# Kernel tuning notes

Hardware: AMD Instinct MI355X
Metric: run time of the kernel (lower is better)

## Reference

```python
import jax, jax.numpy as jnp
import numpy as np

N = 50000   # nodes
E = 800000  # edges
D = 128     # nfeat == nhid
C = 40      # nclass
L = 4       # nlayer
EPS_BN = 1e-5
EPS_PN = 1e-6
PN_SCALE = 1.0


def setup_inputs() -> dict:
    key = jax.random.key(0)
    ks = jax.random.split(key, 10)
    x = jax.random.normal(ks[0], (N, D), jnp.float32)
    edge_row = jax.random.randint(ks[1], (E,), 0, N)   # destination rows of adj
    edge_col = jax.random.randint(ks[2], (E,), 0, N)   # source cols of adj
    edge_val = jax.random.uniform(ks[3], (E,), jnp.float32)
    # BatchNorm1d(nfeat) affine params
    bn_gamma = jnp.ones((D,), jnp.float32)
    bn_beta = jnp.zeros((D,), jnp.float32)
    s = 1.0 / np.sqrt(D)
    fc_in_w = jax.random.uniform(ks[4], (D, D), jnp.float32, -s, s)
    fc_in_b = jax.random.uniform(ks[5], (D,), jnp.float32, -s, s)
    gc_w = jax.random.uniform(ks[6], (L, D, D), jnp.float32, -s, s)
    gc_b = jax.random.uniform(ks[7], (L, D), jnp.float32, -s, s)
    fc_out_w = jax.random.uniform(ks[8], (D, C), jnp.float32, -s, s)
    fc_out_b = jax.random.uniform(ks[9], (C,), jnp.float32, -s, s)
    return dict(x=x, edge_row=edge_row, edge_col=edge_col, edge_val=edge_val,
                bn_gamma=bn_gamma, bn_beta=bn_beta,
                fc_in_w=fc_in_w, fc_in_b=fc_in_b,
                gc_w=gc_w, gc_b=gc_b,
                fc_out_w=fc_out_w, fc_out_b=fc_out_b)


def pair_norm(x):
    # PairNorm 'PN': center columns, scale by sqrt(mean row squared-norm)
    x = x - x.mean(axis=0, keepdims=True)
    rownorm_mean = jnp.sqrt(EPS_PN + jnp.mean(jnp.sum(x * x, axis=1)))
    return PN_SCALE * x / rownorm_mean


def spmm(edge_row, edge_col, edge_val, h):
    # out[i] = sum_{e: row(e)=i} val_e * h[col(e)]  (torch.spmm(adj, h))
    return jax.ops.segment_sum(edge_val[:, None] * h[edge_col], edge_row, num_segments=N)


def reference(x, edge_row, edge_col, edge_val, bn_gamma, bn_beta,
              fc_in_w, fc_in_b, gc_w, gc_b, fc_out_w, fc_out_b):
    x_old = jnp.zeros_like(x)  # zeros_like(input x), shape [N, D]
    # BatchNorm1d over nodes (batch statistics; dropout inactive / eval)
    mu = x.mean(axis=0)
    var = x.var(axis=0)
    x = (x - mu) / jnp.sqrt(var + EPS_BN) * bn_gamma + bn_beta
    x = x @ fc_in_w + fc_in_b
    for i in range(L):
        h = x @ gc_w[i]                                   # [N, D] dense GEMM
        h = spmm(edge_row, edge_col, edge_val, h) + gc_b[i]
        h = jax.nn.relu(pair_norm(h))
        # skip=1 -> i % 1 == 0 always: residual add every layer
        x = h + x_old
        x_old = x
    return x @ fc_out_w + fc_out_b
```

## Files before the change

kernel.cpp:

```cpp
#include <hip/hip_runtime.h>
#include <hip/hip_bf16.h>


constexpr int DD = 128;

struct alignas(16) f4 { float v[4]; };
typedef unsigned short ushort;
typedef unsigned int uint;
typedef short short8 __attribute__((ext_vector_type(8)));
typedef float f32x4 __attribute__((ext_vector_type(4)));

__device__ inline ushort f2bf(float f) {
    uint u = __float_as_uint(f);
    u += 0x7fffu + ((u >> 16) & 1u);
    return (ushort)(u >> 16);
}
__device__ inline void bf8_unpack(uint4 u, float* v) {
    v[0] = __uint_as_float(u.x << 16); v[1] = __uint_as_float(u.x & 0xffff0000u);
    v[2] = __uint_as_float(u.y << 16); v[3] = __uint_as_float(u.y & 0xffff0000u);
    v[4] = __uint_as_float(u.z << 16); v[5] = __uint_as_float(u.z & 0xffff0000u);
    v[6] = __uint_as_float(u.w << 16); v[7] = __uint_as_float(u.w & 0xffff0000u);
}
__device__ inline uint4 bf8_pack(const float* v) {
    uint4 o;
    o.x = (uint)f2bf(v[0]) | ((uint)f2bf(v[1]) << 16);
    o.y = (uint)f2bf(v[2]) | ((uint)f2bf(v[3]) << 16);
    o.z = (uint)f2bf(v[4]) | ((uint)f2bf(v[5]) << 16);
    o.w = (uint)f2bf(v[6]) | ((uint)f2bf(v[7]) << 16);
    return o;
}

__global__ __launch_bounds__(256) void col_reduce_k(const float* __restrict__ X, int n,
    float* __restrict__ psum, float* __restrict__ psq)
{
    int c = threadIdx.x & (DD - 1);
    int half = threadIdx.x >> 7;
    int rows_per_blk = (n + gridDim.x - 1) / gridDim.x;
    int r0 = blockIdx.x * rows_per_blk;
    int r1 = min(n, r0 + rows_per_blk);
    float s = 0.f, ss = 0.f;
    for (int r = r0 + half; r < r1; r += 2) {
        float v = X[(size_t)r * DD + c];
        s += v; ss += v * v;
    }
    __shared__ float ls[256], lq[256];
    ls[threadIdx.x] = s; lq[threadIdx.x] = ss;
    __syncthreads();
    if (half == 0) {
        psum[blockIdx.x * DD + c] = ls[c] + ls[c + 128];
        psq [blockIdx.x * DD + c] = lq[c] + lq[c + 128];
    }
}

template<bool BN>
__global__ __launch_bounds__(1024) void finalize_k(const float* __restrict__ psum,
    const float* __restrict__ psq, int nblk, int n,
    const float* __restrict__ gamma, const float* __restrict__ beta,
    float* __restrict__ AB)
{
    const int c = threadIdx.x & (DD - 1);
    const int g = threadIdx.x >> 7;
    float s = 0.f, ss = 0.f;
    for (int b = g; b < nblk; b += 8) {
        s  += psum[b * DD + c];
        ss += psq [b * DD + c];
    }
    __shared__ float Ls[8][DD], Lq[8][DD];
    Ls[g][c] = s; Lq[g][c] = ss;
    __syncthreads();
    float ts = 0.f, tss = 0.f;
    #pragma unroll
    for (int k = 0; k < 8; k++) { ts += Ls[k][c]; tss += Lq[k][c]; }
    float mu = ts / (float)n;
    if (BN) {
        if (threadIdx.x < DD) {
            float var = tss / (float)n - mu * mu;
            float a = gamma[c] * rsqrtf(var + 1e-5f);
            AB[c] = a;
            AB[DD + c] = beta[c] - mu * a;
        }
    } else {
        float cent = tss - (float)n * mu * mu;
        __syncthreads();
        if (g == 0) Ls[0][c] = cent;
        __syncthreads();
        for (int off = 64; off > 0; off >>= 1) {
            if (threadIdx.x < off) Ls[0][threadIdx.x] += Ls[0][threadIdx.x + off];
            __syncthreads();
        }
        if (threadIdx.x < DD) {
            float inv = rsqrtf(1e-6f + Ls[0][0] / (float)n);
            AB[c] = inv;
            AB[DD + c] = -mu * inv;
        }
    }
}

__global__ __launch_bounds__(256) void weights_k(const float* __restrict__ gc_w,
    const float* __restrict__ fc_in_w, const float* __restrict__ fc_in_b,
    const float* __restrict__ fc_out_w,
    ushort* __restrict__ Wt, ushort* __restrict__ Wtc, ushort* __restrict__ WtO,
    float* __restrict__ bc)
{
    const int b = blockIdx.x;
    const int t = threadIdx.x;
    if (b < 64) {
        int w = b >> 4, tile = b & 15;
        int tr = (tile >> 2) * 32, tc = (tile & 3) * 32;
        const float* W = gc_w + (size_t)w * DD * DD;
        ushort* Wo = Wt + (size_t)w * DD * DD;
        __shared__ float tls[32][33];
        int tx = t & 31, ty = t >> 5;
        #pragma unroll
        for (int j = 0; j < 32; j += 8)
            tls[ty + j][tx] = W[(size_t)(tr + ty + j) * DD + tc + tx];
        __syncthreads();
        #pragma unroll
        for (int j = 0; j < 32; j += 8)
            Wo[(size_t)(tc + ty + j) * DD + (tr + tx)] = f2bf(tls[tx][ty + j]);
    } else if (b == 64) {
        for (int i = t; i < 48 * DD; i += 256) {
            int nn = i >> 7, k = i & 127;
            float v = (nn < 40) ? fc_out_w[(size_t)k * 40 + nn] : 0.f;
            WtO[i] = f2bf(v);
        }
    } else if (b == 65) {
        if (t < DD) {
            float acc = 0.f;
            for (int j = 0; j < DD; j++) acc += fc_in_b[j] * gc_w[(size_t)j * DD + t];
            bc[t] = acc;
        }
    } else {
        int idx = (b - 66) * 256 + t;
        int nn = idx & 127, k = idx >> 7;
        float acc = 0.f;
        for (int j = 0; j < DD; j++)
            acc += fc_in_w[(size_t)k * DD + j] * gc_w[(size_t)j * DD + nn];
        Wtc[(size_t)nn * DD + k] = f2bf(acc);
    }
}

template<int PRE, int NCOLF, int NCOLW, bool BIAS, bool OUTBF, bool WRITEX>
__global__ __launch_bounds__(256) void gemm_mfma_k(const void* __restrict__ INv,
    const ushort* __restrict__ Wt, const float* __restrict__ AB,
    const float* __restrict__ bias, void* __restrict__ Xresv,
    void* __restrict__ Yout, int ystride, int n)
{
    __shared__ short xs[128][136];
    __shared__ short ws[NCOLF * 16][136];
    __shared__ float bias_s[DD];
    const int t = threadIdx.x;
    if (BIAS && t < NCOLW) bias_s[t] = bias[t];

    const int row0 = blockIdx.x * 128;
    if (PRE <= 1) {
        const float* IN = (const float*)INv;
        for (int i = t; i < 128 * 32; i += 256) {
            int m = i >> 5, koff = (i & 31) << 2;
            int r = row0 + m;
            f4 v; v.v[0] = v.v[1] = v.v[2] = v.v[3] = 0.f;
            if (r < n) {
                v = *reinterpret_cast<const f4*>(IN + (size_t)r * DD + koff);
                #pragma unroll
                for (int j = 0; j < 4; j++) v.v[j] = v.v[j] * AB[koff + j] + AB[DD + koff + j];
            }
            uint2 p;
            p.x = (uint)f2bf(v.v[0]) | ((uint)f2bf(v.v[1]) << 16);
            p.y = (uint)f2bf(v.v[2]) | ((uint)f2bf(v.v[3]) << 16);
            *reinterpret_cast<uint2*>(&xs[m][koff]) = p;
        }
    } else {
        const ushort* IN = (const ushort*)INv;
        ushort* Xres = (ushort*)Xresv;
        for (int i = t; i < 128 * 16; i += 256) {
            int m = i >> 4, k8 = (i & 15) << 3;
            int r = row0 + m;
            float v[8];
            if (r < n) {
                uint4 u = *reinterpret_cast<const uint4*>(IN + (size_t)r * DD + k8);
                bf8_unpack(u, v);
                #pragma unroll
                for (int j = 0; j < 8; j++)
                    v[j] = fmaxf(v[j] * AB[k8 + j] + AB[DD + k8 + j], 0.f);
                if (PRE == 3) {
                    uint4 xo = *reinterpret_cast<const uint4*>(Xres + (size_t)r * DD + k8);
                    float xov[8]; bf8_unpack(xo, xov);
                    #pragma unroll
                    for (int j = 0; j < 8; j++) v[j] += xov[j];
                }
                uint4 pk = bf8_pack(v);
                if (WRITEX)
                    *reinterpret_cast<uint4*>(Xres + (size_t)r * DD + k8) = pk;
                *reinterpret_cast<uint4*>(&xs[m][k8]) = pk;
            } else {
                uint4 z; z.x = z.y = z.z = z.w = 0u;
                *reinterpret_cast<uint4*>(&xs[m][k8]) = z;
            }
        }
    }
    for (int i = t; i < NCOLF * 256; i += 256) {
        int nn = i >> 4, koff = (i & 15) << 3;
        *reinterpret_cast<uint4*>(&ws[nn][koff]) =
            *reinterpret_cast<const uint4*>(Wt + (size_t)nn * DD + koff);
    }
    __syncthreads();

    const int wave = t >> 6, lane = t & 63, fr = lane & 15, g = lane >> 4;
    f32x4 acc[2][NCOLF];
    #pragma unroll
    for (int m = 0; m < 2; m++)
        #pragma unroll
        for (int c = 0; c < NCOLF; c++) acc[m][c] = (f32x4){0.f, 0.f, 0.f, 0.f};

    #pragma unroll 2
    for (int ks = 0; ks < 4; ks++) {
        int k0 = ks * 32 + g * 8;
        short8 a0 = *reinterpret_cast<const short8*>(&xs[wave * 32 + fr][k0]);
        short8 a1 = *reinterpret_cast<const short8*>(&xs[wave * 32 + 16 + fr][k0]);
        #pragma unroll
        for (int c = 0; c < NCOLF; c++) {
            short8 b = *reinterpret_cast<const short8*>(&ws[c * 16 + fr][k0]);
            acc[0][c] = __builtin_amdgcn_mfma_f32_16x16x32_bf16(b, a0, acc[0][c], 0, 0, 0);
            acc[1][c] = __builtin_amdgcn_mfma_f32_16x16x32_bf16(b, a1, acc[1][c], 0, 0, 0);
        }
    }

    #pragma unroll
    for (int m = 0; m < 2; m++) {
        const int row = row0 + wave * 32 + m * 16 + fr;
        if (row < n) {
            #pragma unroll
            for (int c = 0; c < NCOLF; c++) {
                int n0 = c * 16 + g * 4;
                if (OUTBF) {
                    float b0 = BIAS ? bias_s[n0 + 0] : 0.f, b1 = BIAS ? bias_s[n0 + 1] : 0.f;
                    float b2 = BIAS ? bias_s[n0 + 2] : 0.f, b3 = BIAS ? bias_s[n0 + 3] : 0.f;
                    uint2 o;
                    o.x = (uint)f2bf(acc[m][c][0] + b0) | ((uint)f2bf(acc[m][c][1] + b1) << 16);
                    o.y = (uint)f2bf(acc[m][c][2] + b2) | ((uint)f2bf(acc[m][c][3] + b3) << 16);
                    *reinterpret_cast<uint2*>((ushort*)Yout + (size_t)row * DD + n0) = o;
                } else if (n0 + 3 < NCOLW) {
                    f4 o;
                    #pragma unroll
                    for (int j = 0; j < 4; j++)
                        o.v[j] = acc[m][c][j] + (BIAS ? bias_s[n0 + j] : 0.f);
                    *reinterpret_cast<f4*>((float*)Yout + (size_t)row * ystride + n0) = o;
                }
            }
        }
    }
}

__global__ __launch_bounds__(256) void hist_k(const int* __restrict__ erow,
    int* __restrict__ deg, int e)
{
    int i = blockIdx.x * 256 + threadIdx.x;
    if (i < e) atomicAdd(&deg[erow[i]], 1);
}

constexpr int SCAN_TILE = 1024;
constexpr int BSH = 9;

__global__ __launch_bounds__(256) void scan1_k(const int* __restrict__ deg,
    int* __restrict__ local, int* __restrict__ bsum, int n)
{
    const int t = threadIdx.x;
    const int base = blockIdx.x * SCAN_TILE + t * 4;
    int v0 = 0, v1 = 0, v2 = 0, v3 = 0;
    if (base + 3 < n) {
        int4 v = *reinterpret_cast<const int4*>(deg + base);
        v0 = v.x; v1 = v.y; v2 = v.z; v3 = v.w;
    } else {
        if (base + 0 < n) v0 = deg[base + 0];
        if (base + 1 < n) v1 = deg[base + 1];
        if (base + 2 < n) v2 = deg[base + 2];
        if (base + 3 < n) v3 = deg[base + 3];
    }
    int s = v0 + v1 + v2 + v3;
    __shared__ int ps[256];
    ps[t] = s;
    __syncthreads();
    for (int off = 1; off < 256; off <<= 1) {
        int add = (t >= off) ? ps[t - off] : 0;
        __syncthreads();
        ps[t] += add;
        __syncthreads();
    }
    int excl = (t > 0) ? ps[t - 1] : 0;
    int o0 = excl, o1 = excl + v0, o2 = o1 + v1, o3 = o2 + v2;
    if (base + 3 < n) {
        int4 o; o.x = o0; o.y = o1; o.z = o2; o.w = o3;
        *reinterpret_cast<int4*>(local + base) = o;
    } else {
        if (base + 0 < n) local[base + 0] = o0;
        if (base + 1 < n) local[base + 1] = o1;
        if (base + 2 < n) local[base + 2] = o2;
        if (base + 3 < n) local[base + 3] = o3;
    }
    if (t == 255) bsum[blockIdx.x] = ps[255];
}

__global__ __launch_bounds__(256) void scan2_k(const int* __restrict__ bsum,
    int* __restrict__ bpre, int nb, int* __restrict__ rowptr, int n)
{
    const int t = threadIdx.x;
    __shared__ int ps[256];
    ps[t] = (t < nb) ? bsum[t] : 0;
    __syncthreads();
    for (int off = 1; off < 256; off <<= 1) {
        int add = (t >= off) ? ps[t - off] : 0;
        __syncthreads();
        ps[t] += add;
        __syncthreads();
    }
    if (t < nb) bpre[t] = (t > 0) ? ps[t - 1] : 0;
    if (t == 255) rowptr[n] = ps[255];
}

__global__ __launch_bounds__(256) void scan3_k(const int* __restrict__ local,
    const int* __restrict__ bpre, int* __restrict__ rowptr, int* __restrict__ cursor,
    int* __restrict__ gcur, int n)
{
    const int base = blockIdx.x * SCAN_TILE + threadIdx.x * 4;
    const int p = bpre[blockIdx.x];
    if (base + 3 < n) {
        int4 v = *reinterpret_cast<const int4*>(local + base);
        v.x += p; v.y += p; v.z += p; v.w += p;
        *reinterpret_cast<int4*>(rowptr + base) = v;
        *reinterpret_cast<int4*>(cursor + base) = v;
        if ((base & 511) == 0) gcur[base >> BSH] = v.x;
    } else {
        #pragma unroll
        for (int j = 0; j < 4; j++)
            if (base + j < n) {
                int v = local[base + j] + p;
                rowptr[base + j] = v;
                cursor[base + j] = v;
                if (((base + j) & 511) == 0) gcur[(base + j) >> BSH] = v;
            }
    }
}

__global__ __launch_bounds__(256) void bin_a_k(const int* __restrict__ erow,
    const int* __restrict__ ecol, const float* __restrict__ evalv,
    int* __restrict__ gcur, uint2* __restrict__ binned, int e)
{
    __shared__ int cnt[128];
    __shared__ int base[128];
    const int t = threadIdx.x;
    if (t < 128) cnt[t] = 0;
    __syncthreads();
    const int i0 = blockIdx.x * 2048 + t * 8;
    int rw[8], cl[8], rk[8];
    float vl[8];
    #pragma unroll
    for (int j = 0; j < 8; j++) {
        int idx = i0 + j;
        if (idx < e) { rw[j] = erow[idx]; cl[j] = ecol[idx]; vl[j] = evalv[idx]; }
        else rw[j] = -1;
    }
    #pragma unroll
    for (int j = 0; j < 8; j++)
        if (rw[j] >= 0) rk[j] = atomicAdd(&cnt[rw[j] >> BSH], 1);
    __syncthreads();
    if (t < 128) base[t] = cnt[t] ? atomicAdd(&gcur[t], cnt[t]) : 0;
    __syncthreads();
    #pragma unroll
    for (int j = 0; j < 8; j++) {
        if (rw[j] >= 0) {
            int b = rw[j] >> BSH, rl = rw[j] & ((1 << BSH) - 1);
            uint2 pr;
            pr.x = (uint)cl[j] | ((uint)rl << 16);
            pr.y = __float_as_uint(vl[j]);
            binned[base[b] + rk[j]] = pr;
        }
    }
}

__global__ __launch_bounds__(256) void bin_b_k(const uint2* __restrict__ binned,
    const int* __restrict__ rowptr, int* __restrict__ cursor,
    int2* __restrict__ cpair, int n)
{
    const int b = blockIdx.x;
    const int r0 = min(b << BSH, n), r1 = min((b + 1) << BSH, n);
    const int p0 = rowptr[r0], p1 = rowptr[r1];
    for (int p = p0 + threadIdx.x; p < p1; p += 256) {
        uint2 u = binned[p];
        int r = (b << BSH) + (int)(u.x >> 16);
        int pos = atomicAdd(&cursor[r], 1);
        int2 pr; pr.x = (int)(u.x & 0xffffu); pr.y = (int)u.y;
        cpair[pos] = pr;
    }
}

__global__ __launch_bounds__(256) void spmm_fused_k(const int* __restrict__ rowptr,
    const int2* __restrict__ cpair, const ushort* __restrict__ H,
    ushort* __restrict__ AGG, float* __restrict__ psum, float* __restrict__ psq, int n)
{
    const int t = threadIdx.x;
    const int gid = blockIdx.x * 256 + t;
    const int r = gid >> 4;
    const int q = t & 15;
    float a[8];
    #pragma unroll
    for (int j = 0; j < 8; j++) a[j] = 0.f;

    if (r < n) {
        int p0 = rowptr[r], p1 = rowptr[r + 1];
        const ushort* Hq = H + q * 8;
        int p = p0;
        for (; p + 8 <= p1; p += 8) {
            int2 c[8];
            #pragma unroll
            for (int j = 0; j < 8; j++) c[j] = cpair[p + j];
            uint4 u[8];
            #pragma unroll
            for (int j = 0; j < 8; j++)
                u[j] = *reinterpret_cast<const uint4*>(Hq + (size_t)c[j].x * DD);
            #pragma unroll
            for (int j = 0; j < 8; j++) {
                float v = __int_as_float(c[j].y);
                a[0] = fmaf(v, __uint_as_float(u[j].x << 16), a[0]);
                a[1] = fmaf(v, __uint_as_float(u[j].x & 0xffff0000u), a[1]);
                a[2] = fmaf(v, __uint_as_float(u[j].y << 16), a[2]);
                a[3] = fmaf(v, __uint_as_float(u[j].y & 0xffff0000u), a[3]);
                a[4] = fmaf(v, __uint_as_float(u[j].z << 16), a[4]);
                a[5] = fmaf(v, __uint_as_float(u[j].z & 0xffff0000u), a[5]);
                a[6] = fmaf(v, __uint_as_float(u[j].w << 16), a[6]);
                a[7] = fmaf(v, __uint_as_float(u[j].w & 0xffff0000u), a[7]);
            }
        }
        if (p + 4 <= p1) {
            int2 c[4];
            #pragma unroll
            for (int j = 0; j < 4; j++) c[j] = cpair[p + j];
            uint4 u[4];
            #pragma unroll
            for (int j = 0; j < 4; j++)
                u[j] = *reinterpret_cast<const uint4*>(Hq + (size_t)c[j].x * DD);
            #pragma unroll
            for (int j = 0; j < 4; j++) {
                float v = __int_as_float(c[j].y);
                a[0] = fmaf(v, __uint_as_float(u[j].x << 16), a[0]);
                a[1] = fmaf(v, __uint_as_float(u[j].x & 0xffff0000u), a[1]);
                a[2] = fmaf(v, __uint_as_float(u[j].y << 16), a[2]);
                a[3] = fmaf(v, __uint_as_float(u[j].y & 0xffff0000u), a[3]);
                a[4] = fmaf(v, __uint_as_float(u[j].z << 16), a[4]);
                a[5] = fmaf(v, __uint_as_float(u[j].z & 0xffff0000u), a[5]);
                a[6] = fmaf(v, __uint_as_float(u[j].w << 16), a[6]);
                a[7] = fmaf(v, __uint_as_float(u[j].w & 0xffff0000u), a[7]);
            }
            p += 4;
        }
        for (; p < p1; p++) {
            int2 cv = cpair[p];
            float v = __int_as_float(cv.y);
            uint4 u = *reinterpret_cast<const uint4*>(Hq + (size_t)cv.x * DD);
            a[0] = fmaf(v, __uint_as_float(u.x << 16), a[0]);
            a[1] = fmaf(v, __uint_as_float(u.x & 0xffff0000u), a[1]);
            a[2] = fmaf(v, __uint_as_float(u.y << 16), a[2]);
            a[3] = fmaf(v, __uint_as_float(u.y & 0xffff0000u), a[3]);
            a[4] = fmaf(v, __uint_as_float(u.z << 16), a[4]);
            a[5] = fmaf(v, __uint_as_float(u.z & 0xffff0000u), a[5]);
            a[6] = fmaf(v, __uint_as_float(u.w << 16), a[6]);
            a[7] = fmaf(v, __uint_as_float(u.w & 0xffff0000u), a[7]);
        }
        *reinterpret_cast<uint4*>(AGG + (size_t)r * DD + q * 8) = bf8_pack(a);
    }

    float s[8], sq[8];
    #pragma unroll
    for (int j = 0; j < 8; j++) { s[j] = a[j]; sq[j] = a[j] * a[j]; }
    #pragma unroll
    for (int j = 0; j < 8; j++) {
        s[j]  += __shfl_xor(s[j], 16);  sq[j] += __shfl_xor(sq[j], 16);
        s[j]  += __shfl_xor(s[j], 32);  sq[j] += __shfl_xor(sq[j], 32);
    }
    __shared__ float sA[4][DD], qA[4][DD];
    const int wave = t >> 6, lane = t & 63;
    if (lane < 16) {
        #pragma unroll
        for (int j = 0; j < 8; j++) {
            sA[wave][lane * 8 + j] = s[j];
            qA[wave][lane * 8 + j] = sq[j];
        }
    }
    __syncthreads();
    if (t < DD) {
        float S = 0.f, Q = 0.f;
        #pragma unroll
        for (int w = 0; w < 4; w++) { S += sA[w][t]; Q += qA[w][t]; }
        int slot = (blockIdx.x & 63) * DD + t;
        atomicAdd(&psum[slot], S);
        atomicAdd(&psq[slot], Q);
    }
}

extern "C" void kernel_launch(void* const* d_in, const int* in_sizes, int n_in,
                              void* d_out, int out_size, void* d_ws, size_t ws_size,
                              hipStream_t stream)
{
    const float* x_in     = (const float*)d_in[0];
    const int*   erow     = (const int*)d_in[1];
    const int*   ecol     = (const int*)d_in[2];
    const float* evalv    = (const float*)d_in[3];
    const float* gamma    = (const float*)d_in[4];
    const float* beta     = (const float*)d_in[5];
    const float* fc_in_w  = (const float*)d_in[6];
    const float* fc_in_b  = (const float*)d_in[7];
    const float* gc_w     = (const float*)d_in[8];
    const float* fc_out_w = (const float*)d_in[10];
    const float* fc_out_b = (const float*)d_in[11];
    float* out = (float*)d_out;

    const int n = in_sizes[0] / DD;
    const int e = in_sizes[1];
    const int NB = 512;
    const int nscan = (n + SCAN_TILE - 1) / SCAN_TILE;
    const int nbuk = (n + (1 << BSH) - 1) >> BSH;

    char* w = (char*)d_ws;
    char* zbase   = w;
    int* deg      = (int*)w;     w += (size_t)(n + 4) * 4;
    float* PSUMS  = (float*)w;   w += (size_t)4 * 64 * DD * 4;
    float* PSQS   = (float*)w;   w += (size_t)4 * 64 * DD * 4;
    const size_t zbytes = (size_t)(w - zbase);
    float* PSUM   = (float*)w;   w += (size_t)NB * DD * 4;
    float* PSQ    = (float*)w;   w += (size_t)NB * DD * 4;
    ushort* X     = (ushort*)w;  w += (size_t)n * DD * 2;
    ushort* Hb    = (ushort*)w;  w += (size_t)n * DD * 2;
    ushort* AGG   = (ushort*)w;  w += (size_t)n * DD * 2;
    float* AB     = (float*)w;   w += 2 * DD * 4;
    ushort* Wt    = (ushort*)w;  w += (size_t)4 * DD * DD * 2;
    ushort* Wtc   = (ushort*)w;  w += (size_t)DD * DD * 2;
    ushort* WtO   = (ushort*)w;  w += (size_t)48 * DD * 2;
    float* bc     = (float*)w;   w += DD * 4;
    int* rowptr   = (int*)w;     w += (size_t)(n + 4) * 4;
    int* cursor   = (int*)w;     w += (size_t)(n + 4) * 4;
    int* slocal   = (int*)w;     w += (size_t)(n + 4) * 4;
    int* bsum     = (int*)w;     w += 1024;
    int* bpre     = (int*)w;     w += 1024;
    int* gcur     = (int*)w;     w += 1024;
    uint2* binned = (uint2*)w;   w += (size_t)e * 8;
    int2* cpair   = (int2*)w;    w += (size_t)e * 8;

    hipMemsetAsync(zbase, 0, zbytes, stream);

    hist_k<<<(e + 255) / 256, 256, 0, stream>>>(erow, deg, e);
    scan1_k<<<nscan, 256, 0, stream>>>(deg, slocal, bsum, n);
    scan2_k<<<1, 256, 0, stream>>>(bsum, bpre, nscan, rowptr, n);
    scan3_k<<<nscan, 256, 0, stream>>>(slocal, bpre, rowptr, cursor, gcur, n);
    bin_a_k<<<(e + 2047) / 2048, 256, 0, stream>>>(erow, ecol, evalv, gcur, binned, e);
    bin_b_k<<<nbuk, 256, 0, stream>>>(binned, rowptr, cursor, cpair, n);

    weights_k<<<130, 256, 0, stream>>>(gc_w, fc_in_w, fc_in_b, fc_out_w, Wt, Wtc, WtO, bc);

    col_reduce_k<<<NB, 256, 0, stream>>>(x_in, n, PSUM, PSQ);
    finalize_k<true><<<1, 1024, 0, stream>>>(PSUM, PSQ, NB, n, gamma, beta, AB);

    const int gblocks128 = (n + 127) / 128;
    const int sblocks = ((size_t)n * 16 + 255) / 256;

    gemm_mfma_k<1, 8, 128, true, true, false><<<gblocks128, 256, 0, stream>>>(
        x_in, Wtc, AB, bc, nullptr, Hb, DD, n);

    for (int l = 0; l < 4; l++) {
        spmm_fused_k<<<sblocks, 256, 0, stream>>>(rowptr, cpair, Hb, AGG,
            PSUMS + (size_t)l * 64 * DD, PSQS + (size_t)l * 64 * DD, n);
        finalize_k<false><<<1, 1024, 0, stream>>>(PSUMS + (size_t)l * 64 * DD,
            PSQS + (size_t)l * 64 * DD, 64, n, nullptr, nullptr, AB);
        if (l < 3) {
            if (l == 0)
                gemm_mfma_k<2, 8, 128, false, true, true><<<gblocks128, 256, 0, stream>>>(
                    AGG, Wt + (size_t)(l + 1) * DD * DD, AB, nullptr, X, Hb, DD, n);
            else
                gemm_mfma_k<3, 8, 128, false, true, true><<<gblocks128, 256, 0, stream>>>(
                    AGG, Wt + (size_t)(l + 1) * DD * DD, AB, nullptr, X, Hb, DD, n);
        } else {
            gemm_mfma_k<3, 3, 40, true, false, false><<<gblocks128, 256, 0, stream>>>(
                AGG, WtO, AB, fc_out_b, X, out, 40, n);
        }
    }
}
```

Before: 390.9 us.

## Store H and AGG in four 32-column slices so SpMM gathers stay cache-resident

Changes the bf16 hidden-feature layout from row-major [N,128] to four column slices of [N,32]. The GEMM epilogue writes into and the prologue reads from this sliced layout. SpMM now launches one grid per slice with 4 threads per row, so each slice (about 3.2 MB) can stay in L2/MALL during the random gathers. The cost is that cpair and rowptr are read four times, rows are gathered in 64-byte rather than 256-byte pieces, and the stats reduction needs more shuffles.

```diff
diff --git a/kernel.cpp b/kernel.cpp
--- a/kernel.cpp
+++ b/kernel.cpp
@@ -152,6 +152,7 @@
     const int t = threadIdx.x;
     if (BIAS && t < NCOLW) bias_s[t] = bias[t];
 
+    const size_t sstride = (size_t)n * 32;
     const int row0 = blockIdx.x * 128;
     if (PRE <= 1) {
         const float* IN = (const float*)INv;
@@ -177,7 +178,8 @@
             int r = row0 + m;
             float v[8];
             if (r < n) {
-                uint4 u = *reinterpret_cast<const uint4*>(IN + (size_t)r * DD + k8);
+                uint4 u = *reinterpret_cast<const uint4*>(
+                    IN + (size_t)(k8 >> 5) * sstride + (size_t)r * 32 + (k8 & 31));
                 bf8_unpack(u, v);
                 #pragma unroll
                 for (int j = 0; j < 8; j++)
@@ -238,7 +240,8 @@
                     uint2 o;
                     o.x = (uint)f2bf(acc[m][c][0] + b0) | ((uint)f2bf(acc[m][c][1] + b1) << 16);
                     o.y = (uint)f2bf(acc[m][c][2] + b2) | ((uint)f2bf(acc[m][c][3] + b3) << 16);
-                    *reinterpret_cast<uint2*>((ushort*)Yout + (size_t)row * DD + n0) = o;
+                    *reinterpret_cast<uint2*>((ushort*)Yout + (size_t)(c >> 1) * sstride
+                        + (size_t)row * 32 + (n0 & 31)) = o;
                 } else if (n0 + 3 < NCOLW) {
                     f4 o;
                     #pragma unroll
@@ -395,19 +398,24 @@
 
 __global__ __launch_bounds__(256) void spmm_fused_k(const int* __restrict__ rowptr,
     const int2* __restrict__ cpair, const ushort* __restrict__ H,
-    ushort* __restrict__ AGG, float* __restrict__ psum, float* __restrict__ psq, int n)
+    ushort* __restrict__ AGG, float* __restrict__ psum, float* __restrict__ psq,
+    int n, int bps)
 {
     const int t = threadIdx.x;
-    const int gid = blockIdx.x * 256 + t;
-    const int r = gid >> 4;
-    const int q = t & 15;
+    const int slice = blockIdx.x / bps;
+    const int blk = blockIdx.x - slice * bps;
+    const int gid = blk * 256 + t;
+    const int r = gid >> 2;
+    const int q = t & 3;
+    const size_t sstride = (size_t)n * 32;
+    const ushort* Hs = H + (size_t)slice * sstride;
     float a[8];
     #pragma unroll
     for (int j = 0; j < 8; j++) a[j] = 0.f;
 
     if (r < n) {
         int p0 = rowptr[r], p1 = rowptr[r + 1];
-        const ushort* Hq = H + q * 8;
+        const ushort* Hq = Hs + q * 8;
         int p = p0;
         for (; p + 8 <= p1; p += 8) {
             int2 c[8];
@@ -416,7 +424,7 @@
             uint4 u[8];
             #pragma unroll
             for (int j = 0; j < 8; j++)
-                u[j] = *reinterpret_cast<const uint4*>(Hq + (size_t)c[j].x * DD);
+                u[j] = *reinterpret_cast<const uint4*>(Hq + (size_t)c[j].x * 32);
             #pragma unroll
             for (int j = 0; j < 8; j++) {
                 float v = __int_as_float(c[j].y);
@@ -437,7 +445,7 @@
             uint4 u[4];
             #pragma unroll
             for (int j = 0; j < 4; j++)
-                u[j] = *reinterpret_cast<const uint4*>(Hq + (size_t)c[j].x * DD);
+                u[j] = *reinterpret_cast<const uint4*>(Hq + (size_t)c[j].x * 32);
             #pragma unroll
             for (int j = 0; j < 4; j++) {
                 float v = __int_as_float(c[j].y);
@@ -455,7 +463,7 @@
         for (; p < p1; p++) {
             int2 cv = cpair[p];
             float v = __int_as_float(cv.y);
-            uint4 u = *reinterpret_cast<const uint4*>(Hq + (size_t)cv.x * DD);
+            uint4 u = *reinterpret_cast<const uint4*>(Hq + (size_t)cv.x * 32);
             a[0] = fmaf(v, __uint_as_float(u.x << 16), a[0]);
             a[1] = fmaf(v, __uint_as_float(u.x & 0xffff0000u), a[1]);
             a[2] = fmaf(v, __uint_as_float(u.y << 16), a[2]);
@@ -465,7 +473,8 @@
             a[6] = fmaf(v, __uint_as_float(u.w << 16), a[6]);
             a[7] = fmaf(v, __uint_as_float(u.w & 0xffff0000u), a[7]);
         }
-        *reinterpret_cast<uint4*>(AGG + (size_t)r * DD + q * 8) = bf8_pack(a);
+        *reinterpret_cast<uint4*>(AGG + (size_t)slice * sstride + (size_t)r * 32 + q * 8)
+            = bf8_pack(a);
     }
 
     float s[8], sq[8];
@@ -473,12 +482,14 @@
     for (int j = 0; j < 8; j++) { s[j] = a[j]; sq[j] = a[j] * a[j]; }
     #pragma unroll
     for (int j = 0; j < 8; j++) {
-        s[j]  += __shfl_xor(s[j], 16);  sq[j] += __shfl_xor(sq[j], 16);
-        s[j]  += __shfl_xor(s[j], 32);  sq[j] += __shfl_xor(sq[j], 32);
-    }
-    __shared__ float sA[4][DD], qA[4][DD];
+        s[j] += __shfl_xor(s[j], 4);   sq[j] += __shfl_xor(sq[j], 4);
+        s[j] += __shfl_xor(s[j], 8);   sq[j] += __shfl_xor(sq[j], 8);
+        s[j] += __shfl_xor(s[j], 16);  sq[j] += __shfl_xor(sq[j], 16);
+        s[j] += __shfl_xor(s[j], 32);  sq[j] += __shfl_xor(sq[j], 32);
+    }
+    __shared__ float sA[4][32], qA[4][32];
     const int wave = t >> 6, lane = t & 63;
-    if (lane < 16) {
+    if (lane < 4) {
         #pragma unroll
         for (int j = 0; j < 8; j++) {
             sA[wave][lane * 8 + j] = s[j];
@@ -486,11 +497,11 @@
         }
     }
     __syncthreads();
-    if (t < DD) {
+    if (t < 32) {
         float S = 0.f, Q = 0.f;
         #pragma unroll
         for (int w = 0; w < 4; w++) { S += sA[w][t]; Q += qA[w][t]; }
-        int slot = (blockIdx.x & 63) * DD + t;
+        int slot = (blockIdx.x & 63) * DD + slice * 32 + t;
         atomicAdd(&psum[slot], S);
         atomicAdd(&psq[slot], Q);
     }
@@ -559,14 +570,15 @@
     finalize_k<true><<<1, 1024, 0, stream>>>(PSUM, PSQ, NB, n, gamma, beta, AB);
 
     const int gblocks128 = (n + 127) / 128;
-    const int sblocks = ((size_t)n * 16 + 255) / 256;
+    const int bps = ((size_t)n * 4 + 255) / 256;
+    const int sblocks = 4 * bps;
 
     gemm_mfma_k<1, 8, 128, true, true, false><<<gblocks128, 256, 0, stream>>>(
         x_in, Wtc, AB, bc, nullptr, Hb, DD, n);
 
     for (int l = 0; l < 4; l++) {
         spmm_fused_k<<<sblocks, 256, 0, stream>>>(rowptr, cpair, Hb, AGG,
-            PSUMS + (size_t)l * 64 * DD, PSQS + (size_t)l * 64 * DD, n);
+            PSUMS + (size_t)l * 64 * DD, PSQS + (size_t)l * 64 * DD, n, bps);
         finalize_k<false><<<1, 1024, 0, stream>>>(PSUMS + (size_t)l * 64 * DD,
             PSQS + (size_t)l * 64 * DD, 64, n, nullptr, nullptr, AB);
         if (l < 3) {
```

Measured after the change: 419.6 us. 7.4% more time.
